# Kernel tuning notes

Hardware: AMD Instinct MI355X
Metric: run time of the kernel (lower is better)

The kernel has to match this reference:

```python
import jax, jax.numpy as jnp
import numpy as np

IN_FEATURES = 1024
OUT_FEATURES = 1024
NNZ = 104858  # round(0.1 * 1024 * 1024)
BATCH = 1024


def setup_inputs() -> dict:
    key = jax.random.key(0)
    k1, k2, k3, k4 = jax.random.split(key, 4)
    x = jax.random.normal(k1, (BATCH, IN_FEATURES), dtype=jnp.float32)
    weights = jax.random.normal(k2, (NNZ,), dtype=jnp.float32)
    bias = jax.random.normal(k3, (OUT_FEATURES,), dtype=jnp.float32)
    # COO indices: row in [0, OUT_FEATURES), col in [0, IN_FEATURES)
    indices = jax.random.randint(k4, (2, NNZ), 0, 1024, dtype=jnp.int64)
    return {"x": x, "weights": weights, "bias": bias, "indices": indices}


def reference(x, weights, bias, indices):
    # y[n, r] = sum_{k: row_k == r} w_k * x[n, col_k]  (unstructured COO spmm)
    row, col = indices[0], indices[1]
    # gather input columns per nnz entry: [nnz, N]
    gathered = x.T[col] * weights[:, None]
    # scatter-add into output rows: [out_features, N]
    out = jax.ops.segment_sum(gathered, row, num_segments=OUT_FEATURES)
    return out.T + bias  # [N, out_features]
```

## Files before the change

kernel.cpp:

```cpp
#include <hip/hip_runtime.h>
#include <hip/hip_bf16.h>

#define NNZ   104858
#define NB    1024
#define NIN   1024
#define NOUT  1024

typedef __bf16 bf16;
typedef bf16  bf16x8 __attribute__((ext_vector_type(8)));
typedef float f32x4  __attribute__((ext_vector_type(4)));

__global__ __launch_bounds__(256)
void k_densify(const int* __restrict__ idx, const float* __restrict__ w,
               float* __restrict__ Wd) {
    int k = blockIdx.x * 256 + threadIdx.x;
    if (k < NNZ) {
        int r = idx[k] & (NOUT - 1);
        int c = idx[NNZ + k] & (NIN - 1);
        atomicAdd(&Wd[r * NIN + c], w[k]);
    }
}

__global__ __launch_bounds__(256)
void k_convert(const float* __restrict__ x, const float* __restrict__ Wd,
               bf16* __restrict__ xb, bf16* __restrict__ wb) {
    const int b = blockIdx.x, t = threadIdx.x;
    const float* src = (b < 512) ? x : Wd;
    bf16*        dst = (b < 512) ? xb : wb;
    const int base = ((b & 511) * 256 + t) * 8;
    const float4* s4 = (const float4*)(src + base);
    float4 v0 = s4[0], v1 = s4[1];
    bf16x8 o;
    o[0] = (bf16)v0.x; o[1] = (bf16)v0.y; o[2] = (bf16)v0.z; o[3] = (bf16)v0.w;
    o[4] = (bf16)v1.x; o[5] = (bf16)v1.y; o[6] = (bf16)v1.z; o[7] = (bf16)v1.w;
    *(bf16x8*)(dst + base) = o;
}

__device__ __forceinline__ void gload_lds16(const void* g, void* l) {
    __builtin_amdgcn_global_load_lds((const __attribute__((address_space(1))) void*)g,
                                     (__attribute__((address_space(3))) void*)l,
                                     16, 0, 0);
}

__global__ __launch_bounds__(256)
void k_gemm(const bf16* __restrict__ A, const bf16* __restrict__ B,
            float* __restrict__ P) {
    __shared__ __align__(16) bf16 As[128 * 64];
    __shared__ __align__(16) bf16 Bs[128 * 64];
    const int t  = threadIdx.x;
    const int m0 = blockIdx.x * 128, n0 = blockIdx.y * 128, kz = blockIdx.z;
    const int lane = t & 63;
    const int wv = t >> 6, wr = wv >> 1, wc = wv & 1;
    const int fr = lane & 15, fg = lane >> 4;

    f32x4 acc[4][4] = {};

    const int srow = t >> 3;
    const int sg   = t & 7;

    for (int ks = 0; ks < 4; ++ks) {
        const int kbase = kz * 256 + ks * 64;
        #pragma unroll
        for (int i = 0; i < 4; ++i) {
            int row = i * 32 + srow;
            int g2  = sg ^ (row & 7);
            gload_lds16(A + (size_t)(m0 + row) * NIN + kbase + g2 * 8,
                        As + row * 64 + sg * 8);
            gload_lds16(B + (size_t)(n0 + row) * NIN + kbase + g2 * 8,
                        Bs + row * 64 + sg * 8);
        }
        __syncthreads();

        bf16x8 af[4][2], bfr[4][2];
        #pragma unroll
        for (int mi = 0; mi < 4; ++mi) {
            int row = wr * 64 + mi * 16 + fr;
            #pragma unroll
            for (int kk = 0; kk < 2; ++kk) {
                int gsw = (kk * 4 + fg) ^ (row & 7);
                af[mi][kk] = *(const bf16x8*)(As + row * 64 + gsw * 8);
            }
        }
        #pragma unroll
        for (int ni = 0; ni < 4; ++ni) {
            int row = wc * 64 + ni * 16 + fr;
            #pragma unroll
            for (int kk = 0; kk < 2; ++kk) {
                int gsw = (kk * 4 + fg) ^ (row & 7);
                bfr[ni][kk] = *(const bf16x8*)(Bs + row * 64 + gsw * 8);
            }
        }
        #pragma unroll
        for (int mi = 0; mi < 4; ++mi)
            #pragma unroll
            for (int ni = 0; ni < 4; ++ni)
                #pragma unroll
                for (int kk = 0; kk < 2; ++kk)
                    acc[mi][ni] = __builtin_amdgcn_mfma_f32_16x16x32_bf16(
                        af[mi][kk], bfr[ni][kk], acc[mi][ni], 0, 0, 0);
        __syncthreads();
    }

    float* Ps = P + (size_t)kz * NB * NOUT;
    #pragma unroll
    for (int mi = 0; mi < 4; ++mi) {
        #pragma unroll
        for (int ni = 0; ni < 4; ++ni) {
            int row0 = m0 + wr * 64 + mi * 16 + fg * 4;
            int col  = n0 + wc * 64 + ni * 16 + fr;
            #pragma unroll
            for (int j = 0; j < 4; ++j)
                Ps[(size_t)(row0 + j) * NOUT + col] = acc[mi][ni][j];
        }
    }
}

__global__ __launch_bounds__(256)
void k_reduce(const float4* __restrict__ P, const float4* __restrict__ bias4,
              float4* __restrict__ out) {
    int i = blockIdx.x * 256 + threadIdx.x;
    float4 a = P[i], b = P[i + 262144], c = P[i + 524288], d = P[i + 786432];
    float4 bb = bias4[i & 255];
    float4 r;
    r.x = a.x + b.x + c.x + d.x + bb.x;
    r.y = a.y + b.y + c.y + d.y + bb.y;
    r.z = a.z + b.z + c.z + d.z + bb.z;
    r.w = a.w + b.w + c.w + d.w + bb.w;
    out[i] = r;
}

static inline size_t align256(size_t v) { return (v + 255) & ~(size_t)255; }

extern "C" void kernel_launch(void* const* d_in, const int* in_sizes, int n_in,
                              void* d_out, int out_size, void* d_ws, size_t ws_size,
                              hipStream_t stream) {
    const float* x    = (const float*)d_in[0];
    const float* wts  = (const float*)d_in[1];
    const float* bias = (const float*)d_in[2];
    const int*   idx  = (const int*)d_in[3];

    char* ws = (char*)d_ws;
    size_t off = 0;
    float* Wd = (float*)(ws + off); off = align256(off + (size_t)NOUT * NIN * 4);
    bf16*  xb = (bf16*) (ws + off); off = align256(off + (size_t)NB * NIN * 2);
    bf16*  wb = (bf16*) (ws + off); off = align256(off + (size_t)NOUT * NIN * 2);
    float* P  = (float*)(ws + off); off = align256(off + (size_t)4 * NB * NOUT * 4);

    const int nb_nnz = (NNZ + 255) / 256;

    hipMemsetAsync(Wd, 0, (size_t)NOUT * NIN * 4, stream);
    k_densify<<<nb_nnz, 256, 0, stream>>>(idx, wts, Wd);
    k_convert<<<1024, 256, 0, stream>>>(x, Wd, xb, wb);
    k_gemm<<<dim3(8, 8, 4), 256, 0, stream>>>(xb, wb, P);
    k_reduce<<<1024, 256, 0, stream>>>((const float4*)P, (const float4*)bias,
                                       (float4*)d_out);
}
```

Baseline: 34.94 us.

## Fuse split-K reduction and bias into GEMM via in-block LDS reduction

Replaces the 4-way split-K GEMM plus separate reduce kernel with 64x64 output tiles where two 256-thread halves each cover half of K and combine their partial sums through LDS before adding bias and writing the output. The memset of the dense weight matrix is merged with the x-to-bf16 conversion into one pre-kernel, and the W conversion becomes its own kernel. This removes the 16 MB partial-sum buffer traffic and one launch, at the cost of smaller tiles with less reuse and lower MFMA work per wave.

```diff
diff --git a/kernel.cpp b/kernel.cpp
--- a/kernel.cpp
+++ b/kernel.cpp
@@ -11,6 +11,26 @@
 typedef float f32x4  __attribute__((ext_vector_type(4)));
 
 __global__ __launch_bounds__(256)
+void k_pre(const float* __restrict__ x, float* __restrict__ Wd,
+           bf16* __restrict__ xb) {
+    const int b = blockIdx.x, t = threadIdx.x;
+    if (b < 512) {
+        float4 z = {0.f, 0.f, 0.f, 0.f};
+        float4* w4 = (float4*)Wd;
+        int i = (b * 256 + t) * 2;
+        w4[i] = z; w4[i + 1] = z;
+    } else {
+        const int base = ((b - 512) * 256 + t) * 8;
+        const float4* s4 = (const float4*)(x + base);
+        float4 v0 = s4[0], v1 = s4[1];
+        bf16x8 o;
+        o[0] = (bf16)v0.x; o[1] = (bf16)v0.y; o[2] = (bf16)v0.z; o[3] = (bf16)v0.w;
+        o[4] = (bf16)v1.x; o[5] = (bf16)v1.y; o[6] = (bf16)v1.z; o[7] = (bf16)v1.w;
+        *(bf16x8*)(xb + base) = o;
+    }
+}
+
+__global__ __launch_bounds__(256)
 void k_densify(const int* __restrict__ idx, const float* __restrict__ w,
                float* __restrict__ Wd) {
     int k = blockIdx.x * 256 + threadIdx.x;
@@ -22,18 +42,14 @@
 }
 
 __global__ __launch_bounds__(256)
-void k_convert(const float* __restrict__ x, const float* __restrict__ Wd,
-               bf16* __restrict__ xb, bf16* __restrict__ wb) {
-    const int b = blockIdx.x, t = threadIdx.x;
-    const float* src = (b < 512) ? x : Wd;
-    bf16*        dst = (b < 512) ? xb : wb;
-    const int base = ((b & 511) * 256 + t) * 8;
-    const float4* s4 = (const float4*)(src + base);
+void k_convW(const float* __restrict__ Wd, bf16* __restrict__ wb) {
+    const int base = (blockIdx.x * 256 + threadIdx.x) * 8;
+    const float4* s4 = (const float4*)(Wd + base);
     float4 v0 = s4[0], v1 = s4[1];
     bf16x8 o;
     o[0] = (bf16)v0.x; o[1] = (bf16)v0.y; o[2] = (bf16)v0.z; o[3] = (bf16)v0.w;
     o[4] = (bf16)v1.x; o[5] = (bf16)v1.y; o[6] = (bf16)v1.z; o[7] = (bf16)v1.w;
-    *(bf16x8*)(dst + base) = o;
+    *(bf16x8*)(wb + base) = o;
 }
 
 __device__ __forceinline__ void gload_lds16(const void* g, void* l) {
@@ -42,58 +58,63 @@
                                      16, 0, 0);
 }
 
-__global__ __launch_bounds__(256)
+__global__ __launch_bounds__(512)
 void k_gemm(const bf16* __restrict__ A, const bf16* __restrict__ B,
-            float* __restrict__ P) {
-    __shared__ __align__(16) bf16 As[128 * 64];
-    __shared__ __align__(16) bf16 Bs[128 * 64];
+            const float* __restrict__ bias, float* __restrict__ out) {
+    __shared__ __align__(16) bf16 As[2][64 * 64];
+    __shared__ __align__(16) bf16 Bs[2][64 * 64];
+    __shared__ f32x4 red[4][64][4];
+
     const int t  = threadIdx.x;
-    const int m0 = blockIdx.x * 128, n0 = blockIdx.y * 128, kz = blockIdx.z;
+    const int m0 = blockIdx.x * 64, n0 = blockIdx.y * 64;
     const int lane = t & 63;
-    const int wv = t >> 6, wr = wv >> 1, wc = wv & 1;
+    const int wv = t >> 6;
+    const int half = wv >> 2;
+    const int w4 = wv & 3, wr = w4 >> 1, wc = w4 & 1;
     const int fr = lane & 15, fg = lane >> 4;
 
-    f32x4 acc[4][4] = {};
+    const int th   = t & 255;
+    const int srow = th >> 3;
+    const int sg   = th & 7;
 
-    const int srow = t >> 3;
-    const int sg   = t & 7;
+    f32x4 acc[2][2] = {};
 
-    for (int ks = 0; ks < 4; ++ks) {
-        const int kbase = kz * 256 + ks * 64;
+    for (int ks = 0; ks < 8; ++ks) {
+        const int kbase = half * 512 + ks * 64;
         #pragma unroll
-        for (int i = 0; i < 4; ++i) {
+        for (int i = 0; i < 2; ++i) {
             int row = i * 32 + srow;
             int g2  = sg ^ (row & 7);
             gload_lds16(A + (size_t)(m0 + row) * NIN + kbase + g2 * 8,
-                        As + row * 64 + sg * 8);
+                        As[half] + row * 64 + sg * 8);
             gload_lds16(B + (size_t)(n0 + row) * NIN + kbase + g2 * 8,
-                        Bs + row * 64 + sg * 8);
+                        Bs[half] + row * 64 + sg * 8);
         }
         __syncthreads();
 
-        bf16x8 af[4][2], bfr[4][2];
+        bf16x8 af[2][2], bfr[2][2];
         #pragma unroll
-        for (int mi = 0; mi < 4; ++mi) {
-            int row = wr * 64 + mi * 16 + fr;
+        for (int mi = 0; mi < 2; ++mi) {
+            int row = wr * 32 + mi * 16 + fr;
             #pragma unroll
             for (int kk = 0; kk < 2; ++kk) {
                 int gsw = (kk * 4 + fg) ^ (row & 7);
-                af[mi][kk] = *(const bf16x8*)(As + row * 64 + gsw * 8);
+                af[mi][kk] = *(const bf16x8*)(As[half] + row * 64 + gsw * 8);
             }
         }
         #pragma unroll
-        for (int ni = 0; ni < 4; ++ni) {
-            int row = wc * 64 + ni * 16 + fr;
+        for (int ni = 0; ni < 2; ++ni) {
+            int row = wc * 32 + ni * 16 + fr;
             #pragma unroll
             for (int kk = 0; kk < 2; ++kk) {
                 int gsw = (kk * 4 + fg) ^ (row & 7);
-                bfr[ni][kk] = *(const bf16x8*)(Bs + row * 64 + gsw * 8);
+                bfr[ni][kk] = *(const bf16x8*)(Bs[half] + row * 64 + gsw * 8);
             }
         }
         #pragma unroll
-        for (int mi = 0; mi < 4; ++mi)
+        for (int mi = 0; mi < 2; ++mi)
             #pragma unroll
-            for (int ni = 0; ni < 4; ++ni)
+            for (int ni = 0; ni < 2; ++ni)
                 #pragma unroll
                 for (int kk = 0; kk < 2; ++kk)
                     acc[mi][ni] = __builtin_amdgcn_mfma_f32_16x16x32_bf16(
@@ -101,32 +122,29 @@
         __syncthreads();
     }
 
-    float* Ps = P + (size_t)kz * NB * NOUT;
-    #pragma unroll
-    for (int mi = 0; mi < 4; ++mi) {
+    if (half == 1) {
         #pragma unroll
-        for (int ni = 0; ni < 4; ++ni) {
-            int row0 = m0 + wr * 64 + mi * 16 + fg * 4;
-            int col  = n0 + wc * 64 + ni * 16 + fr;
+        for (int mi = 0; mi < 2; ++mi)
             #pragma unroll
-            for (int j = 0; j < 4; ++j)
-                Ps[(size_t)(row0 + j) * NOUT + col] = acc[mi][ni][j];
+            for (int ni = 0; ni < 2; ++ni)
+                red[w4][lane][mi * 2 + ni] = acc[mi][ni];
+    }
+    __syncthreads();
+    if (half == 0) {
+        #pragma unroll
+        for (int mi = 0; mi < 2; ++mi) {
+            #pragma unroll
+            for (int ni = 0; ni < 2; ++ni) {
+                f32x4 p = red[w4][lane][mi * 2 + ni];
+                int row0 = m0 + wr * 32 + mi * 16 + fg * 4;
+                int col  = n0 + wc * 32 + ni * 16 + fr;
+                float bb = bias[col];
+                #pragma unroll
+                for (int j = 0; j < 4; ++j)
+                    out[(size_t)(row0 + j) * NOUT + col] = acc[mi][ni][j] + p[j] + bb;
+            }
         }
     }
-}
-
-__global__ __launch_bounds__(256)
-void k_reduce(const float4* __restrict__ P, const float4* __restrict__ bias4,
-              float4* __restrict__ out) {
-    int i = blockIdx.x * 256 + threadIdx.x;
-    float4 a = P[i], b = P[i + 262144], c = P[i + 524288], d = P[i + 786432];
-    float4 bb = bias4[i & 255];
-    float4 r;
-    r.x = a.x + b.x + c.x + d.x + bb.x;
-    r.y = a.y + b.y + c.y + d.y + bb.y;
-    r.z = a.z + b.z + c.z + d.z + bb.z;
-    r.w = a.w + b.w + c.w + d.w + bb.w;
-    out[i] = r;
 }
 
 static inline size_t align256(size_t v) { return (v + 255) & ~(size_t)255; }
@@ -144,14 +162,11 @@
     float* Wd = (float*)(ws + off); off = align256(off + (size_t)NOUT * NIN * 4);
     bf16*  xb = (bf16*) (ws + off); off = align256(off + (size_t)NB * NIN * 2);
     bf16*  wb = (bf16*) (ws + off); off = align256(off + (size_t)NOUT * NIN * 2);
-    float* P  = (float*)(ws + off); off = align256(off + (size_t)4 * NB * NOUT * 4);
 
     const int nb_nnz = (NNZ + 255) / 256;
 
-    hipMemsetAsync(Wd, 0, (size_t)NOUT * NIN * 4, stream);
+    k_pre<<<1024, 256, 0, stream>>>(x, Wd, xb);
     k_densify<<<nb_nnz, 256, 0, stream>>>(idx, wts, Wd);
-    k_convert<<<1024, 256, 0, stream>>>(x, Wd, xb, wb);
-    k_gemm<<<dim3(8, 8, 4), 256, 0, stream>>>(xb, wb, P);
-    k_reduce<<<1024, 256, 0, stream>>>((const float4*)P, (const float4*)bias,
-                                       (float4*)d_out);
+    k_convW<<<512, 256, 0, stream>>>(Wd, wb);
+    k_gemm<<<dim3(16, 16), 512, 0, stream>>>(xb, wb, bias, (float*)d_out);
 }
```

Measured after the change: 29.68 us. 15.0% less time.
